# Performance work log

Measured on AMD Instinct MI355X. Metric: run time of the kernel, lower is better.

## Reference

```python
import jax, jax.numpy as jnp
import numpy as np
import math

B, T, E = 1, 2048, 1024
H = 8                      # num_heads
D = E // H // 2            # head_dim = 64
LAMBDA_INIT = 0.8 - 0.6 * math.exp(-0.3 * 1)  # depth=1
SCALE_BASE = 512.0
THETA = 10000.0


def _rope_tables(T, d):
    # lucidrains rotary-embedding-torch, use_xpos=True, interleaved pairs
    inv_freq = 1.0 / (THETA ** (jnp.arange(0, d, 2, dtype=jnp.float32) / d))
    pos = jnp.arange(T, dtype=jnp.float32)
    freqs = pos[:, None] * inv_freq[None, :]            # (T, d/2)
    freqs = jnp.repeat(freqs, 2, axis=-1)               # (T, d) interleaved
    sv = (jnp.arange(0, d, 2, dtype=jnp.float32) + 0.4 * d) / (1.4 * d)
    power = (pos - T // 2) / SCALE_BASE
    scale = sv[None, :] ** power[:, None]               # (T, d/2)
    scale = jnp.concatenate([scale, scale], axis=-1)    # (T, d)
    return freqs, scale


def _rotate_half(x):
    # interleaved rotate: (..., d) pairs (x1, x2) -> (-x2, x1)
    x1 = x[..., 0::2]
    x2 = x[..., 1::2]
    return jnp.stack([-x2, x1], axis=-1).reshape(x.shape)


def _apply_rope(t, freqs, scale):
    # t: (B, T, h, d); freqs/scale: (T, d) broadcast over heads
    f = freqs[None, :, None, :]
    s = scale[None, :, None, :]
    return t * jnp.cos(f) * s + _rotate_half(t) * jnp.sin(f) * s


def setup_inputs() -> dict:
    key = jax.random.key(0)
    ks = jax.random.split(key, 9)
    w = 0.02
    return {
        "x": jax.random.normal(ks[0], (B, T, E), dtype=jnp.float32),
        "Wq": jax.random.normal(ks[1], (E, E), dtype=jnp.float32) * w,
        "Wk": jax.random.normal(ks[2], (E, E), dtype=jnp.float32) * w,
        "Wv": jax.random.normal(ks[3], (E, E), dtype=jnp.float32) * w,
        "Wo": jax.random.normal(ks[4], (E, E), dtype=jnp.float32) * w,
        "lambda_q1": jax.random.normal(ks[5], (D,), dtype=jnp.float32) * 0.1,
        "lambda_k1": jax.random.normal(ks[6], (D,), dtype=jnp.float32) * 0.1,
        "lambda_q2": jax.random.normal(ks[7], (D,), dtype=jnp.float32) * 0.1,
        "lambda_k2": jax.random.normal(ks[8], (D,), dtype=jnp.float32) * 0.1,
    }


def reference(x, Wq, Wk, Wv, Wo, lambda_q1, lambda_k1, lambda_q2, lambda_k2):
    b, t, e = x.shape
    scaling = D ** -0.5

    q = (x @ Wq.T).reshape(b, t, 2 * H, D)
    k = (x @ Wk.T).reshape(b, t, 2 * H, D)   # n_rep = 1
    v = (x @ Wv.T).reshape(b, t, H, 2 * D)

    freqs, scale = _rope_tables(t, D)
    q = _apply_rope(q, freqs, scale)
    k = _apply_rope(k, freqs, 1.0 / scale)   # xpos: keys use scale**-1

    q = jnp.transpose(q, (0, 2, 1, 3)) * scaling   # (B, 2H, T, D)
    k = jnp.transpose(k, (0, 2, 1, 3))             # (B, 2H, T, D)
    v = jnp.transpose(v, (0, 2, 1, 3))             # (B, H, T, 2D)

    scores = jnp.einsum('bhtd,bhsd->bhts', q, k)
    probs = jax.nn.softmax(scores.astype(jnp.float32), axis=-1).astype(scores.dtype)

    lam1 = jnp.exp(jnp.sum(lambda_q1 * lambda_k1))
    lam2 = jnp.exp(jnp.sum(lambda_q2 * lambda_k2))
    lam = lam1 - lam2 + LAMBDA_INIT

    probs = probs.reshape(b, H, 2, t, t)
    diff = probs[:, :, 0] - lam * probs[:, :, 1]   # (B, H, T, T)

    attn = jnp.einsum('bhts,bhsd->bhtd', diff, v)  # (B, H, T, 2D)
    # RMSNorm (no affine), eps=1e-5
    attn = attn * jax.lax.rsqrt(jnp.mean(attn * attn, axis=-1, keepdims=True) + 1e-5)
    attn = attn * (1.0 - LAMBDA_INIT)

    attn = jnp.transpose(attn, (0, 2, 1, 3)).reshape(b, t, e)
    return attn @ Wo.T
```

## Files before the change

kernel.cpp:

```cpp
#include <hip/hip_runtime.h>
#include <hip/hip_bf16.h>

typedef __hip_bfloat16 bf16;
typedef _Float16 f16;
typedef __attribute__((ext_vector_type(8))) __bf16 bf16x8;
typedef __attribute__((ext_vector_type(8))) _Float16 f16x8;
typedef __attribute__((ext_vector_type(4))) _Float16 f16x4;
typedef __attribute__((ext_vector_type(4))) float floatx4;
typedef __attribute__((ext_vector_type(16))) float floatx16;

#define T_SEQ 2048
#define EMB   1024
#define LAMBDA_INIT 0.35550906759096926f

__device__ __forceinline__ bf16 f2bf(float f) {
  unsigned u;
  __builtin_memcpy(&u, &f, 4);
  u += 0x7FFF + ((u >> 16) & 1);
  unsigned short h = (unsigned short)(u >> 16);
  bf16 r;
  __builtin_memcpy(&r, &h, 2);
  return r;
}

__device__ __forceinline__ void gl_lds16(const void* g, void* l) {
  __builtin_amdgcn_global_load_lds((const __attribute__((address_space(1))) void*)g,
                                   (__attribute__((address_space(3))) void*)l, 16, 0, 0);
}

__device__ __forceinline__ floatx4 mfma_h(f16x8 a, f16x8 b, floatx4 c) {
  return __builtin_amdgcn_mfma_f32_16x16x32_f16(a, b, c, 0, 0, 0);
}
__device__ __forceinline__ floatx16 mfma32_h(f16x8 a, f16x8 b, floatx16 c) {
  return __builtin_amdgcn_mfma_f32_32x32x16_f16(a, b, c, 0, 0, 0);
}
__device__ __forceinline__ floatx16 mfma32_bf(bf16x8 a, bf16x8 b, floatx16 c) {
  return __builtin_amdgcn_mfma_f32_32x32x16_bf16(a, b, c, 0, 0, 0);
}

__global__ __launch_bounds__(256) void convert_kernel(
    const float* __restrict__ x,  const float* __restrict__ wq,
    const float* __restrict__ wk, const float* __restrict__ wv,
    const float* __restrict__ wo,
    f16* __restrict__ xf, f16* __restrict__ wqf, f16* __restrict__ wkf,
    f16* __restrict__ wvf, f16* __restrict__ wof)
{
  int b = blockIdx.x;
  const float* src; f16* dst; long off;
  if      (b < 2048) { src = x;  dst = xf;  off = (long)b * 1024; }
  else if (b < 3072) { src = wq; dst = wqf; off = (long)(b - 2048) * 1024; }
  else if (b < 4096) { src = wk; dst = wkf; off = (long)(b - 3072) * 1024; }
  else if (b < 5120) { src = wv; dst = wvf; off = (long)(b - 4096) * 1024; }
  else               { src = wo; dst = wof; off = (long)(b - 5120) * 1024; }
  long i = off + threadIdx.x * 4;
  float4 v = *(const float4*)(src + i);
  f16x4 o;
  o.x = (f16)v.x; o.y = (f16)v.y; o.z = (f16)v.z; o.w = (f16)v.w;
  *(f16x4*)(dst + i) = o;
}

template <int MODE>
__device__ __forceinline__ void gemm64x128_f16(
    const f16* __restrict__ A_, const f16* __restrict__ B_,
    void* C0v, int K, int ldc, int m0, int n0, char* smem)
{
  f16* As = (f16*)smem;
  f16* Bs = (f16*)(smem + 8192);
  const int tid  = threadIdx.x;
  const int wave = tid >> 6, lane = tid & 63, quad = lane >> 4, l16 = lane & 15;
  const int mo = (wave & 1) << 5;
  const int no = (wave >> 1) << 6;

  floatx4 acc[2][4];
  #pragma unroll
  for (int i = 0; i < 2; i++)
    #pragma unroll
    for (int j = 0; j < 4; j++) { acc[i][j][0]=0.f; acc[i][j][1]=0.f; acc[i][j][2]=0.f; acc[i][j][3]=0.f; }

  const int srow = tid >> 3;
  const int ch   = (tid & 7) ^ (srow & 7);
  const long aoff = (long)(m0 + srow) * K + ch * 8;
  const long boff = (long)(n0 + srow) * K + ch * 8;
  const int wb = wave << 10;

  for (int k0 = 0; k0 < K; k0 += 64) {
    #pragma unroll
    for (int rr = 0; rr < 2; rr++)
      gl_lds16(A_ + aoff + k0 + (long)rr * 32 * K, smem + wb + rr * 4096);
    #pragma unroll
    for (int rr = 0; rr < 4; rr++)
      gl_lds16(B_ + boff + k0 + (long)rr * 32 * K, smem + 8192 + wb + rr * 4096);
    __syncthreads();
    #pragma unroll
    for (int kt = 0; kt < 2; kt++) {
      f16x8 a[2], b[4];
      #pragma unroll
      for (int i = 0; i < 2; i++) {
        int m = mo + i * 16 + l16;
        a[i] = *(const f16x8*)(As + m * 64 + ((((kt << 2) | quad) ^ (m & 7)) << 3));
      }
      #pragma unroll
      for (int j = 0; j < 4; j++) {
        int n = no + j * 16 + l16;
        b[j] = *(const f16x8*)(Bs + n * 64 + ((((kt << 2) | quad) ^ (n & 7)) << 3));
      }
      #pragma unroll
      for (int i = 0; i < 2; i++)
        #pragma unroll
        for (int j = 0; j < 4; j++)
          acc[i][j] = mfma_h(a[i], b[j], acc[i][j]);
    }
    __syncthreads();
  }

  if (MODE == 1) {
    #pragma unroll
    for (int i = 0; i < 2; i++)
      #pragma unroll
      for (int j = 0; j < 4; j++)
        #pragma unroll
        for (int r = 0; r < 4; r++) {
          int row = m0 + mo + i * 16 + quad * 4 + r;
          int col = n0 + no + j * 16 + l16;
          ((float*)C0v)[(long)row * ldc + col] = acc[i][j][r];
        }
  } else {
    unsigned short* E = (unsigned short*)smem;
    #pragma unroll
    for (int i = 0; i < 2; i++)
      #pragma unroll
      for (int j = 0; j < 4; j++)
        #pragma unroll
        for (int r = 0; r < 4; r++) {
          int row = mo + i * 16 + quad * 4 + r;
          int col = no + j * 16 + l16;
          float v = acc[i][j][r];
          unsigned short bits;
          if (MODE == 0) {
            bf16 t = f2bf(v);
            __builtin_memcpy(&bits, &t, 2);
          } else {
            float p = __shfl_xor(v, 1, 64);
            int d = col & 63;
            float fr = (float)(m0 + row) * __expf((float)(d >> 1) * -0.28782313662425574f);
            float sn, cs;
            sincosf(fr, &sn, &cs);
            float rot = (col & 1) ? fmaf(v, cs, p * sn) : fmaf(v, cs, -p * sn);
            float power = (float)(m0 + row - 1024) * (1.0f / 512.0f);
            if (MODE == 3) power = -power;
            float sv = fmaf(2.0f, (float)(d & 31), 25.6f) * (1.0f / 89.6f);
            float s = __expf(power * __logf(sv));
            float ov = rot * s;
            if (MODE == 2) ov *= 0.125f;
            f16 t = (f16)ov;
            __builtin_memcpy(&bits, &t, 2);
          }
          E[row * 128 + col] = bits;
        }
    __syncthreads();
    const int rr0 = tid >> 4;
    const int c8  = (tid & 15) * 8;
    #pragma unroll
    for (int p2 = 0; p2 < 4; p2++) {
      int row = p2 * 16 + rr0;
      *(uint4*)((unsigned short*)C0v + (long)(m0 + row) * ldc + n0 + c8) =
          *(const uint4*)(E + row * 128 + c8);
    }
  }
}

__global__ __launch_bounds__(256) void qkv_gemm(
    const f16* __restrict__ xf,
    const f16* __restrict__ wqf, const f16* __restrict__ wkf,
    const f16* __restrict__ wvf,
    f16* __restrict__ qf, f16* __restrict__ kf, bf16* __restrict__ vt)
{
  __shared__ char smem[24576];
  int bid = blockIdx.x;
  if (bid < 256) {
    gemm64x128_f16<2>(xf, wqf, qf, 1024, 1024, (bid >> 3) * 64, (bid & 7) * 128, smem);
  } else if (bid < 512) {
    bid -= 256;
    gemm64x128_f16<3>(xf, wkf, kf, 1024, 1024, (bid >> 3) * 64, (bid & 7) * 128, smem);
  } else {
    bid -= 512;
    gemm64x128_f16<0>(wvf, xf, vt, 1024, 2048, (bid >> 4) * 64, (bid & 15) * 128, smem);
  }
}

__global__ __launch_bounds__(256) void out_gemm(const f16* __restrict__ attn,
                                                const f16* __restrict__ Wo,
                                                float* __restrict__ out)
{
  __shared__ char smem[24576];
  gemm64x128_f16<1>(attn, Wo, out, 1024, 1024,
                    (blockIdx.x >> 3) * 64, (blockIdx.x & 7) * 128, smem);
}

__global__ __launch_bounds__(256) void diff_attn(
    const f16* __restrict__ qf_, const f16* __restrict__ kf_,
    const bf16* __restrict__ vt,
    const float* __restrict__ lq1, const float* __restrict__ lk1,
    const float* __restrict__ lq2, const float* __restrict__ lk2,
    f16* __restrict__ attn)
{
  __shared__ char smem[40960];
  bf16* Vs = (bf16*)(smem + 16384);

  const int tid  = threadIdx.x;
  const int wave = tid >> 6, lane = tid & 63;
  const int l32 = lane & 31, lh = lane >> 5;
  const int h  = blockIdx.x & 7;
  const int qb = blockIdx.x >> 3;
  const int hl = wave >> 1;
  const int ws = wave & 1;
  const int hh = h * 2 + hl;
  const int t0 = qb * 32;

  float a1 = lq1[lane] * lk1[lane];
  float a2 = lq2[lane] * lk2[lane];
  #pragma unroll
  for (int off = 1; off < 64; off <<= 1) {
    a1 += __shfl_xor(a1, off, 64);
    a2 += __shfl_xor(a2, off, 64);
  }
  const float lam = __expf(a1) - __expf(a2) + LAMBDA_INIT;

  f16x8 qfr[4];
  {
    const f16* qrow = qf_ + (long)(t0 + l32) * EMB + hh * 64 + lh * 8;
    #pragma unroll
    for (int kt = 0; kt < 4; kt++) qfr[kt] = *(const f16x8*)(qrow + kt * 16);
  }

  floatx16 o[4];
  #pragma unroll
  for (int nt = 0; nt < 4; nt++)
    #pragma unroll
    for (int r = 0; r < 16; r++) o[nt][r] = 0.f;
  float lr[16];
  #pragma unroll
  for (int r = 0; r < 16; r++) lr[r] = 0.f;

  const int srow = lane >> 3;
  const int ch   = (lane & 7) ^ srow;
  const f16*  kgp = kf_ + (long)(h * 2 + (wave & 1)) * 64 + (long)srow * EMB + ch * 8;
  const bf16* vgp = vt + (long)(h * 128 + (wave - 2) * 64 + srow) * T_SEQ + ch * 8;
  char* ldstK = smem + wave * 8192;
  char* ldstV = smem + 16384 + (wave - 2) * 8192;

  bf16* Pw = (bf16*)(smem + 32768) + wave * 1024;

  for (int kb = 0; kb < T_SEQ; kb += 64) {
    if (wave < 2) {
      #pragma unroll
      for (int j = 0; j < 8; j++)
        gl_lds16(kgp + (long)kb * EMB + (long)j * 8 * EMB, ldstK + j * 1024);
    } else {
      #pragma unroll
      for (int j = 0; j < 8; j++)
        gl_lds16(vgp + kb + (long)j * 8 * T_SEQ, ldstV + j * 1024);
    }
    __syncthreads();

    const f16* Ks = (const f16*)(smem + hl * 8192);
    floatx16 s;
    #pragma unroll
    for (int r = 0; r < 16; r++) s[r] = 0.f;
    #pragma unroll
    for (int kt = 0; kt < 4; kt++) {
      int krow = ws * 32 + l32;
      int c = kt * 2 + lh;
      f16x8 kfr = *(const f16x8*)(Ks + krow * 64 + ((c ^ (krow & 7)) << 3));
      s = mfma32_h(qfr[kt], kfr, s);
    }
    #pragma unroll
    for (int r = 0; r < 16; r++) {
      float pv = __builtin_amdgcn_exp2f(
          fmaf(s[r], 1.4426950408889634f, -17.312340490667562f));
      s[r] = pv;
      lr[r] += pv;
    }
    #pragma unroll
    for (int r = 0; r < 16; r++) {
      int m = (r & 3) + 8 * (r >> 2) + 4 * lh;
      Pw[m * 32 + (((l32 >> 3) ^ ((m >> 1) & 3)) << 3) + (l32 & 7)] = f2bf(s[r]);
    }
    __asm__ volatile("s_waitcnt lgkmcnt(0)" ::: "memory");
    bf16x8 pf[2];
    #pragma unroll
    for (int kt = 0; kt < 2; kt++) {
      int c = kt * 2 + lh;
      pf[kt] = *(const bf16x8*)(Pw + l32 * 32 + ((c ^ ((l32 >> 1) & 3)) << 3));
    }
    #pragma unroll
    for (int nt = 0; nt < 4; nt++) {
      #pragma unroll
      for (int kt = 0; kt < 2; kt++) {
        int vrow = nt * 32 + l32;
        int c = ws * 4 + kt * 2 + lh;
        bf16x8 vf = *(const bf16x8*)(Vs + vrow * 64 + ((c ^ (vrow & 7)) << 3));
        o[nt] = mfma32_bf(pf[kt], vf, o[nt]);
      }
    }
    __syncthreads();
  }

  #pragma unroll
  for (int r = 0; r < 16; r++) {
    lr[r] += __shfl_xor(lr[r], 1, 64);
    lr[r] += __shfl_xor(lr[r], 2, 64);
    lr[r] += __shfl_xor(lr[r], 4, 64);
    lr[r] += __shfl_xor(lr[r], 8, 64);
    lr[r] += __shfl_xor(lr[r], 16, 64);
  }

  float* Cb = (float*)smem;
  float* Lb = (float*)(smem + 32768);

  if (ws == 1) {
    #pragma unroll
    for (int r = 0; r < 16; r++) {
      int m = (r & 3) + 8 * (r >> 2) + 4 * lh;
      #pragma unroll
      for (int nt = 0; nt < 4; nt++)
        Cb[hl * 4096 + m * 128 + nt * 32 + l32] = o[nt][r];
      if (l32 == 0) Lb[hl * 32 + m] = lr[r];
    }
  }
  __syncthreads();
  if (ws == 0) {
    #pragma unroll
    for (int r = 0; r < 16; r++) {
      int m = (r & 3) + 8 * (r >> 2) + 4 * lh;
      float inv = 1.0f / (lr[r] + Lb[hl * 32 + m]);
      #pragma unroll
      for (int nt = 0; nt < 4; nt++)
        o[nt][r] = (o[nt][r] + Cb[hl * 4096 + m * 128 + nt * 32 + l32]) * inv;
    }
  }
  __syncthreads();
  if (hl == 1 && ws == 0) {
    #pragma unroll
    for (int r = 0; r < 16; r++) {
      int m = (r & 3) + 8 * (r >> 2) + 4 * lh;
      #pragma unroll
      for (int nt = 0; nt < 4; nt++)
        Cb[4096 + m * 128 + nt * 32 + l32] = o[nt][r];
    }
  }
  __syncthreads();
  if (hl == 0 && ws == 0) {
    float ss[16];
    #pragma unroll
    for (int r = 0; r < 16; r++) {
      int m = (r & 3) + 8 * (r >> 2) + 4 * lh;
      ss[r] = 0.f;
      #pragma unroll
      for (int nt = 0; nt < 4; nt++) {
        float v = o[nt][r] - lam * Cb[4096 + m * 128 + nt * 32 + l32];
        o[nt][r] = v;
        ss[r] += v * v;
      }
    }
    #pragma unroll
    for (int r = 0; r < 16; r++) {
      ss[r] += __shfl_xor(ss[r], 1, 64);
      ss[r] += __shfl_xor(ss[r], 2, 64);
      ss[r] += __shfl_xor(ss[r], 4, 64);
      ss[r] += __shfl_xor(ss[r], 8, 64);
      ss[r] += __shfl_xor(ss[r], 16, 64);
      float rms = rsqrtf(ss[r] * (1.0f / 128.0f) + 1e-5f) * (1.0f - LAMBDA_INIT);
      int m = (r & 3) + 8 * (r >> 2) + 4 * lh;
      #pragma unroll
      for (int nt = 0; nt < 4; nt++)
        attn[(long)(t0 + m) * EMB + h * 128 + nt * 32 + l32] = (f16)(o[nt][r] * rms);
    }
  }
}

extern "C" void kernel_launch(void* const* d_in, const int* in_sizes, int n_in,
                              void* d_out, int out_size, void* d_ws, size_t ws_size,
                              hipStream_t stream)
{
  (void)in_sizes; (void)n_in; (void)out_size; (void)ws_size;
  const float* x   = (const float*)d_in[0];
  const float* Wq  = (const float*)d_in[1];
  const float* Wk  = (const float*)d_in[2];
  const float* Wv  = (const float*)d_in[3];
  const float* Wo  = (const float*)d_in[4];
  const float* lq1 = (const float*)d_in[5];
  const float* lk1 = (const float*)d_in[6];
  const float* lq2 = (const float*)d_in[7];
  const float* lk2 = (const float*)d_in[8];
  float* out = (float*)d_out;

  const size_t TM = (size_t)T_SEQ * EMB;
  const size_t WM = (size_t)EMB * EMB;
  bf16* vtws = (bf16*)d_ws;
  f16*  aws  = (f16*)(vtws + TM);
  f16*  xf   = aws  + TM;
  f16*  wqf  = xf   + TM;
  f16*  wkf  = wqf  + WM;
  f16*  wvf  = wkf  + WM;
  f16*  wof  = wvf  + WM;
  f16*  qf   = wof  + WM;
  f16*  kf   = qf   + TM;

  convert_kernel<<<6144, 256, 0, stream>>>(x, Wq, Wk, Wv, Wo,
                                           xf, wqf, wkf, wvf, wof);
  qkv_gemm<<<768, 256, 0, stream>>>(xf, wqf, wkf, wvf, qf, kf, vtws);
  diff_attn<<<512, 256, 0, stream>>>(qf, kf, vtws, lq1, lk1, lq2, lk2, aws);
  out_gemm<<<256, 256, 0, stream>>>(aws, wof, out);
}
```

Measured before the change: 179.2 us.

## Double-buffer K/V tiles and keep P in registers via permlane swaps

Double-buffers the K/V LDS tiles so the next key block's global-to-LDS load is issued before the current block is computed. A vmcnt wait plus a raw barrier replaces the two __syncthreads per iteration. The score MFMA is transposed so each lane holds one query row, which lets P be packed to bf16 with v_cvt_pk_bf16_f32 and permlane32 swaps instead of a round trip through LDS. Row sums become one scalar per lane, removing the per-row shuffle reductions. LDS use grows to 64KB, which may lower occupancy.

Result: faster. 173.5 us (-3.2%).

```diff
diff --git a/kernel.cpp b/kernel.cpp
--- a/kernel.cpp
+++ b/kernel.cpp
@@ -21,6 +21,16 @@
   bf16 r;
   __builtin_memcpy(&r, &h, 2);
   return r;
+}
+
+__device__ __forceinline__ int cvtpk_bf16(float lo, float hi) {
+  int r;
+  asm("v_cvt_pk_bf16_f32 %0, %1, %2" : "=v"(r) : "v"(lo), "v"(hi));
+  return r;
+}
+
+__device__ __forceinline__ void permswap(int& a, int& b) {
+  asm volatile("v_permlane32_swap_b32 %0, %1" : "+v"(a), "+v"(b));
 }
 
 __device__ __forceinline__ void gl_lds16(const void* g, void* l) {
@@ -204,9 +214,7 @@
     const float* __restrict__ lq2, const float* __restrict__ lk2,
     f16* __restrict__ attn)
 {
-  __shared__ char smem[40960];
-  bf16* Vs = (bf16*)(smem + 16384);
-
+  __shared__ char smem[65536];
   const int tid  = threadIdx.x;
   const int wave = tid >> 6, lane = tid & 63;
   const int l32 = lane & 31, lh = lane >> 5;
@@ -238,32 +246,50 @@
   for (int nt = 0; nt < 4; nt++)
     #pragma unroll
     for (int r = 0; r < 16; r++) o[nt][r] = 0.f;
-  float lr[16];
-  #pragma unroll
-  for (int r = 0; r < 16; r++) lr[r] = 0.f;
+  float lr = 0.f;
 
   const int srow = lane >> 3;
   const int ch   = (lane & 7) ^ srow;
-  const f16*  kgp = kf_ + (long)(h * 2 + (wave & 1)) * 64 + (long)srow * EMB + ch * 8;
+  const f16*  kgp = kf_ + (long)(h * 2 + ws) * 64 + (long)srow * EMB + ch * 8;
   const bf16* vgp = vt + (long)(h * 128 + (wave - 2) * 64 + srow) * T_SEQ + ch * 8;
-  char* ldstK = smem + wave * 8192;
-  char* ldstV = smem + 16384 + (wave - 2) * 8192;
-
-  bf16* Pw = (bf16*)(smem + 32768) + wave * 1024;
+  const int kofs = wave * 8192;
+  const int vofs = 16384 + (wave - 2) * 8192;
+
+  if (wave < 2) {
+    #pragma unroll
+    for (int j = 0; j < 8; j++)
+      gl_lds16(kgp + (long)j * 8 * EMB, smem + kofs + j * 1024);
+  } else {
+    #pragma unroll
+    for (int j = 0; j < 8; j++)
+      gl_lds16(vgp + (long)j * 8 * T_SEQ, smem + vofs + j * 1024);
+  }
 
   for (int kb = 0; kb < T_SEQ; kb += 64) {
-    if (wave < 2) {
-      #pragma unroll
-      for (int j = 0; j < 8; j++)
-        gl_lds16(kgp + (long)kb * EMB + (long)j * 8 * EMB, ldstK + j * 1024);
+    const int cur = (kb >> 6) & 1;
+    const char* sb = smem + cur * 32768;
+    if (kb + 64 < T_SEQ) {
+      char* nb = smem + (cur ^ 1) * 32768;
+      if (wave < 2) {
+        #pragma unroll
+        for (int j = 0; j < 8; j++)
+          gl_lds16(kgp + (long)(kb + 64) * EMB + (long)j * 8 * EMB,
+                   nb + kofs + j * 1024);
+      } else {
+        #pragma unroll
+        for (int j = 0; j < 8; j++)
+          gl_lds16(vgp + (kb + 64) + (long)j * 8 * T_SEQ,
+                   nb + vofs + j * 1024);
+      }
+      asm volatile("s_waitcnt vmcnt(8)" ::: "memory");
     } else {
-      #pragma unroll
-      for (int j = 0; j < 8; j++)
-        gl_lds16(vgp + kb + (long)j * 8 * T_SEQ, ldstV + j * 1024);
-    }
-    __syncthreads();
-
-    const f16* Ks = (const f16*)(smem + hl * 8192);
+      asm volatile("s_waitcnt vmcnt(0)" ::: "memory");
+    }
+    asm volatile("s_barrier" ::: "memory");
+
+    const f16*  Ks  = (const f16*)(sb + hl * 8192);
+    const bf16* Vsb = (const bf16*)(sb + 16384);
+
     floatx16 s;
     #pragma unroll
     for (int r = 0; r < 16; r++) s[r] = 0.f;
@@ -272,26 +298,28 @@
       int krow = ws * 32 + l32;
       int c = kt * 2 + lh;
       f16x8 kfr = *(const f16x8*)(Ks + krow * 64 + ((c ^ (krow & 7)) << 3));
-      s = mfma32_h(qfr[kt], kfr, s);
+      s = mfma32_h(kfr, qfr[kt], s);
     }
     #pragma unroll
     for (int r = 0; r < 16; r++) {
       float pv = __builtin_amdgcn_exp2f(
           fmaf(s[r], 1.4426950408889634f, -17.312340490667562f));
       s[r] = pv;
-      lr[r] += pv;
-    }
-    #pragma unroll
-    for (int r = 0; r < 16; r++) {
-      int m = (r & 3) + 8 * (r >> 2) + 4 * lh;
-      Pw[m * 32 + (((l32 >> 3) ^ ((m >> 1) & 3)) << 3) + (l32 & 7)] = f2bf(s[r]);
-    }
-    __asm__ volatile("s_waitcnt lgkmcnt(0)" ::: "memory");
+      lr += pv;
+    }
     bf16x8 pf[2];
     #pragma unroll
     for (int kt = 0; kt < 2; kt++) {
-      int c = kt * 2 + lh;
-      pf[kt] = *(const bf16x8*)(Pw + l32 * 32 + ((c ^ ((l32 >> 1) & 3)) << 3));
+      const int b0 = kt * 8;
+      int w0 = cvtpk_bf16(s[b0 + 0], s[b0 + 1]);
+      int w1 = cvtpk_bf16(s[b0 + 2], s[b0 + 3]);
+      int w2 = cvtpk_bf16(s[b0 + 4], s[b0 + 5]);
+      int w3 = cvtpk_bf16(s[b0 + 6], s[b0 + 7]);
+      permswap(w0, w2);
+      permswap(w1, w3);
+      union { int i[4]; bf16x8 v; } u;
+      u.i[0] = w0; u.i[1] = w1; u.i[2] = w2; u.i[3] = w3;
+      pf[kt] = u.v;
     }
     #pragma unroll
     for (int nt = 0; nt < 4; nt++) {
@@ -299,21 +327,14 @@
       for (int kt = 0; kt < 2; kt++) {
         int vrow = nt * 32 + l32;
         int c = ws * 4 + kt * 2 + lh;
-        bf16x8 vf = *(const bf16x8*)(Vs + vrow * 64 + ((c ^ (vrow & 7)) << 3));
+        bf16x8 vf = *(const bf16x8*)(Vsb + vrow * 64 + ((c ^ (vrow & 7)) << 3));
         o[nt] = mfma32_bf(pf[kt], vf, o[nt]);
       }
     }
-    __syncthreads();
-  }
-
-  #pragma unroll
-  for (int r = 0; r < 16; r++) {
-    lr[r] += __shfl_xor(lr[r], 1, 64);
-    lr[r] += __shfl_xor(lr[r], 2, 64);
-    lr[r] += __shfl_xor(lr[r], 4, 64);
-    lr[r] += __shfl_xor(lr[r], 8, 64);
-    lr[r] += __shfl_xor(lr[r], 16, 64);
-  }
+    asm volatile("s_barrier" ::: "memory");
+  }
+
+  float lrw = lr + __shfl_xor(lr, 32, 64);
 
   float* Cb = (float*)smem;
   float* Lb = (float*)(smem + 32768);
@@ -325,15 +346,15 @@
       #pragma unroll
       for (int nt = 0; nt < 4; nt++)
         Cb[hl * 4096 + m * 128 + nt * 32 + l32] = o[nt][r];
-      if (l32 == 0) Lb[hl * 32 + m] = lr[r];
-    }
-  }
+    }
+  }
+  if (lh == 0) Lb[ws * 64 + hl * 32 + l32] = lrw;
   __syncthreads();
   if (ws == 0) {
     #pragma unroll
     for (int r = 0; r < 16; r++) {
       int m = (r & 3) + 8 * (r >> 2) + 4 * lh;
-      float inv = 1.0f / (lr[r] + Lb[hl * 32 + m]);
+      float inv = 1.0f / (Lb[hl * 32 + m] + Lb[64 + hl * 32 + m]);
       #pragma unroll
       for (int nt = 0; nt < 4; nt++)
         o[nt][r] = (o[nt][r] + Cb[hl * 4096 + m * 128 + nt * 32 + l32]) * inv;
```
